# Kernel optimization log

Measured on AMD Instinct MI355X. Metric: run time of the kernel, lower is better.

## Reference

```python
import jax, jax.numpy as jnp
import numpy as np

NUM_NODES = 1_000_000
MEM_DIM = 100
TIME_DIM = 100
MSG_DIM = 4
OUT_CH = 2
BATCH = 262144
BN_EPS = 1e-5


def setup_inputs() -> dict:
    key = jax.random.key(0)
    ks = jax.random.split(key, 24)
    s = 0.05
    D = MEM_DIM
    gru_in = 2 * D + MSG_DIM + TIME_DIM  # IdentityMessage output dim = 304
    inp = {
        "n_id": jax.random.randint(ks[0], (BATCH,), 0, NUM_NODES, dtype=jnp.int64 if jax.config.jax_enable_x64 else jnp.int32),
        "memory": jax.random.normal(ks[1], (NUM_NODES, D), jnp.float32),
        "last_update": jax.random.randint(ks[2], (NUM_NODES,), 0, 100000),
        "store_src": jax.random.randint(ks[3], (NUM_NODES,), 0, NUM_NODES),
        "store_dst": jax.random.randint(ks[4], (NUM_NODES,), 0, NUM_NODES),
        "store_t": jax.random.randint(ks[5], (NUM_NODES,), 0, 200000),
        "store_msg": jax.random.normal(ks[6], (NUM_NODES, MSG_DIM), jnp.float32),
        # TimeEncoder: Linear(1, time_dim) followed by cos
        "time_w": jax.random.normal(ks[7], (TIME_DIM, 1), jnp.float32) * s,
        "time_b": jax.random.normal(ks[8], (TIME_DIM,), jnp.float32) * s,
        # GRUCell(input=304, hidden=100)
        "W_ih": jax.random.normal(ks[9], (3 * D, gru_in), jnp.float32) * s,
        "b_ih": jax.random.normal(ks[10], (3 * D,), jnp.float32) * s,
        "W_hh": jax.random.normal(ks[11], (3 * D, D), jnp.float32) * s,
        "b_hh": jax.random.normal(ks[12], (3 * D,), jnp.float32) * s,
        # classifier: Linear(100,64) -> ReLU -> BatchNorm1d(64) -> Linear(64,2)
        "W1": jax.random.normal(ks[13], (64, D), jnp.float32) * s,
        "b1": jax.random.normal(ks[14], (64,), jnp.float32) * s,
        "gamma": jnp.ones((64,), jnp.float32),
        "beta": jnp.zeros((64,), jnp.float32),
        "W2": jax.random.normal(ks[15], (OUT_CH, 64), jnp.float32) * s,
        "b2": jax.random.normal(ks[16], (OUT_CH,), jnp.float32) * s,
    }
    return inp


def reference(n_id, memory, last_update, store_src, store_dst, store_t, store_msg,
              time_w, time_b, W_ih, b_ih, W_hh, b_hh, W1, b1, gamma, beta, W2, b2):
    D = memory.shape[1]
    # ---- TGNMemory._get_updated_memory(n_id) with LastAggregator ----
    h = memory[n_id]                                   # [B, D] gather of node memory
    src = store_src[n_id]
    dst = store_dst[n_id]
    raw_msg = store_msg[n_id]                          # [B, msg_dim]
    dt = (store_t[n_id] - last_update[n_id]).astype(jnp.float32)[:, None]  # [B, 1]
    t_enc = jnp.cos(dt @ time_w.T + time_b)            # [B, time_dim]
    # IdentityMessage: concat(mem[src], mem[dst], raw_msg, time_enc)
    x = jnp.concatenate([memory[src], memory[dst], raw_msg, t_enc], axis=-1)  # [B, 2D+msg+T]
    # GRUCell update
    gi = x @ W_ih.T + b_ih                             # [B, 3D]
    gh = h @ W_hh.T + b_hh                             # [B, 3D]
    i_r, i_z, i_n = gi[:, :D], gi[:, D:2 * D], gi[:, 2 * D:]
    h_r, h_z, h_n = gh[:, :D], gh[:, D:2 * D], gh[:, 2 * D:]
    r = jax.nn.sigmoid(i_r + h_r)
    z = jax.nn.sigmoid(i_z + h_z)
    n = jnp.tanh(i_n + r * h_n)
    h_new = (1.0 - z) * n + z * h                      # [B, D]
    # ---- classifier: Linear -> ReLU -> BatchNorm1d (train stats) -> Linear ----
    a = jax.nn.relu(h_new @ W1.T + b1)                 # [B, 64]
    mu = jnp.mean(a, axis=0)
    var = jnp.var(a, axis=0)
    a = (a - mu) * jax.lax.rsqrt(var + BN_EPS) * gamma + beta
    return a @ W2.T + b2                               # [B, out_channels]
```

## Files before the change

### kernel.cpp

```cpp
#include <hip/hip_runtime.h>
#include <stdint.h>

#define BATCH   262144
#define DMEM    100
#define AS      456

typedef float    f32x4 __attribute__((ext_vector_type(4)));
typedef _Float16 f16x8 __attribute__((ext_vector_type(8)));
typedef unsigned short u16x4 __attribute__((ext_vector_type(4)));

__device__ __forceinline__ unsigned short f2h(float f) {
  union { _Float16 h; unsigned short u; } v; v.h = (_Float16)f;
  return v.u;
}
__device__ __forceinline__ float h2f(unsigned short u) {
  union { _Float16 h; unsigned short u; } v; v.u = u; return (float)v.h;
}

#define MFMA16(A, B, C) __builtin_amdgcn_mfma_f32_16x16x32_f16((A), (B), (C), 0, 0, 0)

__global__ void prep_kernel(const float* __restrict__ W_ih, const float* __restrict__ W_hh,
                            const float* __restrict__ W1,
                            const float* __restrict__ b_ih, const float* __restrict__ b_hh,
                            unsigned short* __restrict__ Bfrag,
                            unsigned short* __restrict__ W1frag,
                            float* __restrict__ biasbuf,
                            float* __restrict__ stats_g) {
  int blk = blockIdx.x;
  int tid = threadIdx.x;
  if (blk == 72) {
    if (tid < 128) stats_g[tid] = 0.f;
    if (tid < 100) {
      biasbuf[tid]       = b_ih[tid]       + b_hh[tid];
      biasbuf[100 + tid] = b_ih[100 + tid] + b_hh[100 + tid];
      biasbuf[200 + tid] = b_ih[200 + tid];
      biasbuf[300 + tid] = b_hh[200 + tid];
    }
    return;
  }
  int o = blk * 4 + (tid >> 6);
  if (o >= 286) return;
  int lane = tid & 63, quad = lane >> 4, l15 = lane & 15;
  if (o < 270) {
    int kc, nt;
    if (o < 190) { kc = o / 19; nt = o % 19; }
    else { int o2 = o - 190; kc = 10 + o2 / 20; int p = o2 % 20; nt = (p < 13) ? p : p + 6; }
    int col = nt * 16 + l15;
    unsigned short* dst = Bfrag + (size_t)o * 512 + lane * 8;
    for (int j = 0; j < 8; ++j) {
      int kg = kc * 32 + quad * 8 + j;
      float v = 0.f;
      if (kc < 10) {
        if (kg < 304 && col < 300) v = W_ih[col * 304 + kg];
      } else {
        int kl = kg - 320;
        if (nt < 13) { if (kl < 100 && col < 200) v = W_hh[col * 100 + kl]; }
        else { int hd = col - 304; if (kl < 100 && hd < 100) v = W_hh[(200 + hd) * 100 + kl]; }
      }
      dst[j] = f2h(v);
    }
  } else {
    int o1 = o - 270;
    int kc = o1 >> 2, nt = o1 & 3;
    int col = nt * 16 + l15;
    unsigned short* dst = W1frag + (size_t)o1 * 512 + lane * 8;
    for (int j = 0; j < 8; ++j) {
      int kg = kc * 32 + quad * 8 + j;
      dst[j] = f2h((kg < 100) ? W1[col * 100 + kg] : 0.f);
    }
  }
}

__global__ __launch_bounds__(256, 2)
void main_kernel(const int* __restrict__ n_id, const float* __restrict__ memory,
                 const int* __restrict__ last_update,
                 const int* __restrict__ store_src, const int* __restrict__ store_dst,
                 const int* __restrict__ store_t, const float* __restrict__ store_msg,
                 const float* __restrict__ time_w, const float* __restrict__ time_b,
                 const float* __restrict__ b1,
                 const unsigned short* __restrict__ Bfrag,
                 const unsigned short* __restrict__ W1frag,
                 const float* __restrict__ biasbuf,
                 unsigned short* __restrict__ a_ws, float* __restrict__ stats_g) {
  __shared__ __align__(16) unsigned short A_lds[64 * AS];
  __shared__ __align__(16) unsigned short hbuf[64 * 100];
  __shared__ float stats[128];

  const int tid  = threadIdx.x;
  const int wave = tid >> 6;
  const int lane = tid & 63;
  const int quad = lane >> 4;
  const int l15  = lane & 15;
  const int wi   = wave >> 1;
  const int wj   = wave & 1;
  const int blk  = blockIdx.x;

  if (tid < 128) stats[tid] = 0.f;

  {
    const int r = tid >> 2;
    const int p = tid & 3;
    const int b = blk * 64 + r;
    const int n = n_id[b];
    const int sidx = store_src[n];
    const int didx = store_dst[n];
    const float dtf = (float)(store_t[n] - last_update[n]);
    const float* ms = memory + (size_t)sidx * DMEM;
    const float* md = memory + (size_t)didx * DMEM;
    const float* mh = memory + (size_t)n * DMEM;
    unsigned short* Ar = A_lds + r * AS;

    f32x4 vals[19];
    int   offs[19];
    #pragma unroll
    for (int i = 0; i < 19; ++i) {
      const int v = i * 4 + p;
      const int a = v / 25;
      const int c = v - a * 25;
      const float* bp = (a == 0) ? ms : ((a == 1) ? md : mh);
      vals[i] = *(const f32x4*)(bp + c * 4);
      offs[i] = (a == 0) ? (c * 4)
              : ((a == 1) ? (100 + c * 4)
              : ((a == 2) ? (320 + c * 4) : 448));
    }
    #pragma unroll
    for (int i = 0; i < 19; ++i) {
      u16x4 h4 = { f2h(vals[i][0]), f2h(vals[i][1]), f2h(vals[i][2]), f2h(vals[i][3]) };
      *(u16x4*)(Ar + offs[i]) = h4;
    }

    const int d0 = p * 25;
    for (int i = 0; i < 25; ++i) {
      const int d = d0 + i;
      Ar[204 + d] = f2h(cosf(dtf * time_w[d] + time_b[d]));
    }

    if (p == 0) {
      f32x4 mg = *(const f32x4*)(store_msg + (size_t)n * 4);
      u16x4 m4 = { f2h(mg[0]), f2h(mg[1]), f2h(mg[2]), f2h(mg[3]) };
      *(u16x4*)(Ar + 200) = m4;
    } else if (p == 1) {
      uint4 z4 = {0u, 0u, 0u, 0u};
      *(uint4*)(Ar + 304) = z4;
      *(uint4*)(Ar + 312) = z4;
    } else if (p == 2) {
      u16x4 z = {0, 0, 0, 0};
      *(u16x4*)(Ar + 420) = z; *(u16x4*)(Ar + 424) = z;
      *(u16x4*)(Ar + 428) = z; *(u16x4*)(Ar + 432) = z;
    } else {
      u16x4 z = {0, 0, 0, 0};
      *(u16x4*)(Ar + 436) = z; *(u16x4*)(Ar + 440) = z; *(u16x4*)(Ar + 444) = z;
    }
  }

  f32x4 acc[13][2];
  #pragma unroll
  for (int t = 0; t < 13; ++t)
    for (int m = 0; m < 2; ++m) acc[t][m] = f32x4{0.f, 0.f, 0.f, 0.f};

  __syncthreads();

  const unsigned short* Arow0 = A_lds + (wi * 32 + l15) * AS;
  const unsigned short* Arow1 = Arow0 + 16 * AS;
  const size_t boff = (size_t)lane * 8;

  if (wj == 0) {
    #pragma unroll 2
    for (int kc = 0; kc < 10; ++kc) {
      const int kb = kc * 32 + quad * 8;
      f16x8 af0 = __builtin_bit_cast(f16x8, *(const uint4*)(Arow0 + kb));
      f16x8 af1 = __builtin_bit_cast(f16x8, *(const uint4*)(Arow1 + kb));
      const unsigned short* Bp = Bfrag + (size_t)(kc * 19) * 512 + boff;
      #pragma unroll
      for (int t = 0; t < 10; ++t) {
        f16x8 bfr = *(const f16x8*)(Bp + (size_t)(2 * t) * 512);
        acc[t][0] = MFMA16(af0, bfr, acc[t][0]);
        acc[t][1] = MFMA16(af1, bfr, acc[t][1]);
      }
    }
    #pragma unroll 2
    for (int kc = 10; kc < 14; ++kc) {
      const int kb = kc * 32 + quad * 8;
      f16x8 af0 = __builtin_bit_cast(f16x8, *(const uint4*)(Arow0 + kb));
      f16x8 af1 = __builtin_bit_cast(f16x8, *(const uint4*)(Arow1 + kb));
      const unsigned short* Bp = Bfrag + (size_t)(190 + (kc - 10) * 20) * 512 + boff;
      #pragma unroll
      for (int t = 0; t < 10; ++t) {
        const int p  = 2 * t;
        const int tl = (p < 13) ? (p >> 1) : ((p + 6) >> 1);
        f16x8 bfr = *(const f16x8*)(Bp + (size_t)p * 512);
        acc[tl][0] = MFMA16(af0, bfr, acc[tl][0]);
        acc[tl][1] = MFMA16(af1, bfr, acc[tl][1]);
      }
    }
  } else {
    #pragma unroll 2
    for (int kc = 0; kc < 10; ++kc) {
      const int kb = kc * 32 + quad * 8;
      f16x8 af0 = __builtin_bit_cast(f16x8, *(const uint4*)(Arow0 + kb));
      f16x8 af1 = __builtin_bit_cast(f16x8, *(const uint4*)(Arow1 + kb));
      const unsigned short* Bp = Bfrag + (size_t)(kc * 19) * 512 + boff;
      #pragma unroll
      for (int t = 0; t < 9; ++t) {
        f16x8 bfr = *(const f16x8*)(Bp + (size_t)(2 * t + 1) * 512);
        acc[t][0] = MFMA16(af0, bfr, acc[t][0]);
        acc[t][1] = MFMA16(af1, bfr, acc[t][1]);
      }
    }
    #pragma unroll 2
    for (int kc = 10; kc < 14; ++kc) {
      const int kb = kc * 32 + quad * 8;
      f16x8 af0 = __builtin_bit_cast(f16x8, *(const uint4*)(Arow0 + kb));
      f16x8 af1 = __builtin_bit_cast(f16x8, *(const uint4*)(Arow1 + kb));
      const unsigned short* Bp = Bfrag + (size_t)(190 + (kc - 10) * 20) * 512 + boff;
      #pragma unroll
      for (int t = 0; t < 10; ++t) {
        const int p  = 2 * t + 1;
        const int tl = (p < 13) ? (p >> 1) : ((p + 6) >> 1);
        f16x8 bfr = *(const f16x8*)(Bp + (size_t)p * 512);
        acc[tl][0] = MFMA16(af0, bfr, acc[tl][0]);
        acc[tl][1] = MFMA16(af1, bfr, acc[tl][1]);
      }
    }
  }
  __syncthreads();

  for (int i = 0; i < 25; ++i) {
    int e = tid + 256 * i;
    hbuf[e] = A_lds[(e / 100) * AS + 320 + (e % 100)];
  }
  __syncthreads();

  #pragma unroll
  for (int t = 0; t < 13; ++t) {
    int col = (t * 2 + wj) * 16 + l15;
    #pragma unroll
    for (int m = 0; m < 2; ++m) {
      int rbase = wi * 32 + m * 16 + quad * 4;
      #pragma unroll
      for (int rr = 0; rr < 4; ++rr)
        A_lds[(rbase + rr) * AS + col] = f2h(acc[t][m][rr]);
    }
  }
  __syncthreads();

  for (int i = 0; i < 25; ++i) {
    int e = tid + 256 * i;
    int r = e / 100, d = e % 100;
    const unsigned short* Gr = A_lds + r * AS;
    float s_r = h2f(Gr[d])       + biasbuf[d];
    float s_z = h2f(Gr[100 + d]) + biasbuf[100 + d];
    float i_n = h2f(Gr[200 + d]) + biasbuf[200 + d];
    float h_n = h2f(Gr[304 + d]) + biasbuf[300 + d];
    float h   = h2f(hbuf[r * 100 + d]);
    float rg = 1.f / (1.f + __expf(-s_r));
    float zg = 1.f / (1.f + __expf(-s_z));
    float nn = tanhf(i_n + rg * h_n);
    float hw = (1.f - zg) * nn + zg * h;
    A_lds[r * AS + d] = f2h(hw);
  }
  __syncthreads();

  f32x4 aacc[2][2];
  #pragma unroll
  for (int m = 0; m < 2; ++m)
    for (int t = 0; t < 2; ++t) aacc[m][t] = f32x4{0.f, 0.f, 0.f, 0.f};
  for (int k4 = 0; k4 < 4; ++k4) {
    int kb = k4 * 32 + quad * 8;
    f16x8 a0 = __builtin_bit_cast(f16x8, *(const uint4*)(Arow0 + kb));
    f16x8 a1 = __builtin_bit_cast(f16x8, *(const uint4*)(Arow1 + kb));
    #pragma unroll
    for (int t = 0; t < 2; ++t) {
      int nt = wj * 2 + t;
      f16x8 bfr = *(const f16x8*)(W1frag + (size_t)(k4 * 4 + nt) * 512 + boff);
      aacc[0][t] = MFMA16(a0, bfr, aacc[0][t]);
      aacc[1][t] = MFMA16(a1, bfr, aacc[1][t]);
    }
  }

  float ssum[2] = {0.f, 0.f}, ssq[2] = {0.f, 0.f};
  #pragma unroll
  for (int t = 0; t < 2; ++t) {
    int col = (wj * 2 + t) * 16 + l15;
    float bb = b1[col];
    #pragma unroll
    for (int m = 0; m < 2; ++m) {
      int rbase = wi * 32 + m * 16 + quad * 4;
      #pragma unroll
      for (int rr = 0; rr < 4; ++rr) {
        float v = fmaxf(aacc[m][t][rr] + bb, 0.f);
        ssum[t] += v; ssq[t] += v * v;
        a_ws[(size_t)(blk * 64 + rbase + rr) * 64 + col] = f2h(v);
      }
    }
  }
  #pragma unroll
  for (int t = 0; t < 2; ++t) {
    ssum[t] += __shfl_xor(ssum[t], 16); ssum[t] += __shfl_xor(ssum[t], 32);
    ssq[t]  += __shfl_xor(ssq[t], 16);  ssq[t]  += __shfl_xor(ssq[t], 32);
  }
  if (quad == 0) {
    #pragma unroll
    for (int t = 0; t < 2; ++t) {
      int col = (wj * 2 + t) * 16 + l15;
      atomicAdd(&stats[col], ssum[t]);
      atomicAdd(&stats[64 + col], ssq[t]);
    }
  }
  __syncthreads();
  if (tid < 128) atomicAdd(&stats_g[tid], stats[tid]);
}

__global__ __launch_bounds__(256)
void out_kernel(const unsigned short* __restrict__ a_ws, const float* __restrict__ stats_g,
                const float* __restrict__ gamma, const float* __restrict__ beta,
                const float* __restrict__ W2, const float* __restrict__ b2,
                float* __restrict__ out) {
  __shared__ float w0[64], w1[64], cpart[128];
  __shared__ float C0s, C1s;
  int tid = threadIdx.x;
  if (tid < 64) {
    const float invB = 1.f / (float)BATCH;
    float mu  = stats_g[tid] * invB;
    float var = stats_g[64 + tid] * invB - mu * mu;
    float g   = gamma[tid] * rsqrtf(var + 1e-5f);
    w0[tid] = g * W2[tid];
    w1[tid] = g * W2[64 + tid];
    float t = beta[tid] - mu * g;
    cpart[tid]      = t * W2[tid];
    cpart[64 + tid] = t * W2[64 + tid];
  }
  __syncthreads();
  if (tid == 0) {
    float c0 = b2[0], c1 = b2[1];
    for (int j = 0; j < 64; ++j) { c0 += cpart[j]; c1 += cpart[64 + j]; }
    C0s = c0; C1s = c1;
  }
  __syncthreads();
  int b = blockIdx.x * 256 + tid;
  const uint4* ap = (const uint4*)(a_ws + (size_t)b * 64);
  float o0 = C0s, o1 = C1s;
  #pragma unroll
  for (int i = 0; i < 8; ++i) {
    uint4 v = ap[i];
    unsigned int uu[4] = {v.x, v.y, v.z, v.w};
    #pragma unroll
    for (int q = 0; q < 4; ++q) {
      float lo = h2f((unsigned short)(uu[q] & 0xffffu));
      float hi = h2f((unsigned short)(uu[q] >> 16));
      int j = i * 8 + q * 2;
      o0 += lo * w0[j] + hi * w0[j + 1];
      o1 += lo * w1[j] + hi * w1[j + 1];
    }
  }
  *(float2*)(out + (size_t)b * 2) = make_float2(o0, o1);
}

extern "C" void kernel_launch(void* const* d_in, const int* in_sizes, int n_in,
                              void* d_out, int out_size, void* d_ws, size_t ws_size,
                              hipStream_t stream) {
  const int*   n_id   = (const int*)d_in[0];
  const float* memory = (const float*)d_in[1];
  const int*   last_u = (const int*)d_in[2];
  const int*   s_src  = (const int*)d_in[3];
  const int*   s_dst  = (const int*)d_in[4];
  const int*   s_t    = (const int*)d_in[5];
  const float* s_msg  = (const float*)d_in[6];
  const float* time_w = (const float*)d_in[7];
  const float* time_b = (const float*)d_in[8];
  const float* W_ih   = (const float*)d_in[9];
  const float* b_ih   = (const float*)d_in[10];
  const float* W_hh   = (const float*)d_in[11];
  const float* b_hh   = (const float*)d_in[12];
  const float* W1     = (const float*)d_in[13];
  const float* b1     = (const float*)d_in[14];
  const float* gamma  = (const float*)d_in[15];
  const float* beta   = (const float*)d_in[16];
  const float* W2     = (const float*)d_in[17];
  const float* b2     = (const float*)d_in[18];

  char* ws = (char*)d_ws;
  float*          stats_g = (float*)ws;
  float*          biasbuf = (float*)(ws + 512);
  unsigned short* Bfrag   = (unsigned short*)(ws + 4096);
  unsigned short* W1frag  = (unsigned short*)(ws + 4096 + 276480);
  unsigned short* a_ws    = (unsigned short*)(ws + (1u << 20));

  prep_kernel<<<73, 256, 0, stream>>>(W_ih, W_hh, W1, b_ih, b_hh, Bfrag, W1frag,
                                      biasbuf, stats_g);
  main_kernel<<<4096, 256, 0, stream>>>(n_id, memory, last_u, s_src, s_dst, s_t,
                                        s_msg, time_w, time_b, b1,
                                        Bfrag, W1frag, biasbuf, a_ws, stats_g);
  out_kernel<<<1024, 256, 0, stream>>>(a_ws, stats_g, gamma, beta, W2, b2, (float*)d_out);
}
```

Before: 829.5 us.

## Repartition GRU GEMM across waves by N-tiles with B-fragment register prefetch

Replaces the 2x2 wave tiling of the fused GRU GEMM with a per-wave set of N-tiles covering all 64 rows, so each A fragment is reused across 4 row tiles. B fragments are software-prefetched one K-chunk ahead in registers, and the classifier GEMM likewise gives each wave one output column tile with W1 fragments preloaded. Biases are staged in LDS, and tanh/sigmoid use fast exp plus reciprocal. The larger accumulator footprint (28 f32x4) and the prefetch buffers raise register pressure at 2 blocks per CU, and the wave load is uneven (one wave has 5 tiles).

```diff
diff --git a/kernel.cpp b/kernel.cpp
--- a/kernel.cpp
+++ b/kernel.cpp
@@ -18,6 +18,15 @@
 }
 
 #define MFMA16(A, B, C) __builtin_amdgcn_mfma_f32_16x16x32_f16((A), (B), (C), 0, 0, 0)
+
+namespace wcfg {
+constexpr int NT[4][7] = {
+  {0, 1, 2, 3, 19, 20, 21},
+  {4, 5, 6, 7, 22, 23, 24},
+  {8, 9, 10, 11, 13, 13, 13},
+  {12, 14, 15, 16, 17, 18, 25}};
+constexpr int LEN[4] = {7, 7, 5, 7};
+}
 
 __global__ void prep_kernel(const float* __restrict__ W_ih, const float* __restrict__ W_hh,
                             const float* __restrict__ W1,
@@ -71,6 +80,110 @@
   }
 }
 
+template<int W>
+__device__ __forceinline__ void b_prefetch0(f16x8 (&bq)[7],
+    const unsigned short* __restrict__ Bfrag, size_t boff) {
+  constexpr auto& NT = wcfg::NT[W];
+  constexpr int L = wcfg::LEN[W];
+  #pragma unroll
+  for (int t = 0; t < 7; ++t)
+    if (t < L && NT[t] < 19)
+      bq[t] = *(const f16x8*)(Bfrag + (size_t)NT[t] * 512 + boff);
+}
+
+template<int W>
+__device__ __forceinline__ void gemm_core(f32x4 (&acc)[7][4], f16x8 (&bq)[7],
+    const unsigned short* __restrict__ Bfrag, const unsigned short* Arow,
+    int quad, size_t boff) {
+  constexpr auto& NT = wcfg::NT[W];
+  constexpr int L = wcfg::LEN[W];
+  #pragma unroll
+  for (int kc = 0; kc < 10; ++kc) {
+    const int kb = kc * 32 + quad * 8;
+    f16x8 af[4];
+    #pragma unroll
+    for (int m = 0; m < 4; ++m)
+      af[m] = __builtin_bit_cast(f16x8, *(const uint4*)(Arow + m * 16 * AS + kb));
+    f16x8 bn[7];
+    if (kc < 9) {
+      const unsigned short* Bk = Bfrag + (size_t)(kc + 1) * 19 * 512 + boff;
+      #pragma unroll
+      for (int t = 0; t < 7; ++t)
+        if (t < L && NT[t] < 19)
+          bn[t] = *(const f16x8*)(Bk + (size_t)NT[t] * 512);
+    } else {
+      const unsigned short* Bk = Bfrag + (size_t)190 * 512 + boff;
+      #pragma unroll
+      for (int t = 0; t < 7; ++t)
+        if (t < L && (NT[t] < 13 || NT[t] >= 19))
+          bn[t] = *(const f16x8*)(Bk + (size_t)((NT[t] < 13) ? NT[t] : NT[t] - 6) * 512);
+    }
+    #pragma unroll
+    for (int t = 0; t < 7; ++t)
+      if (t < L && NT[t] < 19) {
+        #pragma unroll
+        for (int m = 0; m < 4; ++m)
+          acc[t][m] = MFMA16(af[m], bq[t], acc[t][m]);
+      }
+    if (kc < 9) {
+      #pragma unroll
+      for (int t = 0; t < 7; ++t)
+        if (t < L && NT[t] < 19) bq[t] = bn[t];
+    } else {
+      #pragma unroll
+      for (int t = 0; t < 7; ++t)
+        if (t < L && (NT[t] < 13 || NT[t] >= 19)) bq[t] = bn[t];
+    }
+  }
+  #pragma unroll
+  for (int kc = 10; kc < 14; ++kc) {
+    const int kb = kc * 32 + quad * 8;
+    f16x8 af[4];
+    #pragma unroll
+    for (int m = 0; m < 4; ++m)
+      af[m] = __builtin_bit_cast(f16x8, *(const uint4*)(Arow + m * 16 * AS + kb));
+    f16x8 bn[7];
+    if (kc < 13) {
+      const unsigned short* Bk = Bfrag + (size_t)(190 + (kc - 9) * 20) * 512 + boff;
+      #pragma unroll
+      for (int t = 0; t < 7; ++t)
+        if (t < L && (NT[t] < 13 || NT[t] >= 19))
+          bn[t] = *(const f16x8*)(Bk + (size_t)((NT[t] < 13) ? NT[t] : NT[t] - 6) * 512);
+    }
+    #pragma unroll
+    for (int t = 0; t < 7; ++t)
+      if (t < L && (NT[t] < 13 || NT[t] >= 19)) {
+        #pragma unroll
+        for (int m = 0; m < 4; ++m)
+          acc[t][m] = MFMA16(af[m], bq[t], acc[t][m]);
+      }
+    if (kc < 13) {
+      #pragma unroll
+      for (int t = 0; t < 7; ++t)
+        if (t < L && (NT[t] < 13 || NT[t] >= 19)) bq[t] = bn[t];
+    }
+  }
+}
+
+template<int W>
+__device__ __forceinline__ void dump_acc(const f32x4 (&acc)[7][4],
+    unsigned short* A_lds, int quad, int l15) {
+  constexpr auto& NT = wcfg::NT[W];
+  constexpr int L = wcfg::LEN[W];
+  #pragma unroll
+  for (int t = 0; t < 7; ++t)
+    if (t < L) {
+      const int col = NT[t] * 16 + l15;
+      #pragma unroll
+      for (int m = 0; m < 4; ++m) {
+        const int rbase = m * 16 + quad * 4;
+        #pragma unroll
+        for (int rr = 0; rr < 4; ++rr)
+          A_lds[(rbase + rr) * AS + col] = f2h(acc[t][m][rr]);
+      }
+    }
+}
+
 __global__ __launch_bounds__(256, 2)
 void main_kernel(const int* __restrict__ n_id, const float* __restrict__ memory,
                  const int* __restrict__ last_update,
@@ -84,6 +197,7 @@
                  unsigned short* __restrict__ a_ws, float* __restrict__ stats_g) {
   __shared__ __align__(16) unsigned short A_lds[64 * AS];
   __shared__ __align__(16) unsigned short hbuf[64 * 100];
+  __shared__ float bias_lds[400];
   __shared__ float stats[128];
 
   const int tid  = threadIdx.x;
@@ -91,11 +205,14 @@
   const int lane = tid & 63;
   const int quad = lane >> 4;
   const int l15  = lane & 15;
-  const int wi   = wave >> 1;
-  const int wj   = wave & 1;
   const int blk  = blockIdx.x;
+  const size_t boff = (size_t)lane * 8;
 
   if (tid < 128) stats[tid] = 0.f;
+  if (tid < 200) {
+    bias_lds[tid]       = biasbuf[tid];
+    bias_lds[200 + tid] = biasbuf[200 + tid];
+  }
 
   {
     const int r = tid >> 2;
@@ -104,14 +221,14 @@
     const int n = n_id[b];
     const int sidx = store_src[n];
     const int didx = store_dst[n];
-    const float dtf = (float)(store_t[n] - last_update[n]);
+    const int stt  = store_t[n];
+    const int lu   = last_update[n];
     const float* ms = memory + (size_t)sidx * DMEM;
     const float* md = memory + (size_t)didx * DMEM;
     const float* mh = memory + (size_t)n * DMEM;
     unsigned short* Ar = A_lds + r * AS;
 
     f32x4 vals[19];
-    int   offs[19];
     #pragma unroll
     for (int i = 0; i < 19; ++i) {
       const int v = i * 4 + p;
@@ -119,24 +236,17 @@
       const int c = v - a * 25;
       const float* bp = (a == 0) ? ms : ((a == 1) ? md : mh);
       vals[i] = *(const f32x4*)(bp + c * 4);
-      offs[i] = (a == 0) ? (c * 4)
-              : ((a == 1) ? (100 + c * 4)
-              : ((a == 2) ? (320 + c * 4) : 448));
-    }
-    #pragma unroll
-    for (int i = 0; i < 19; ++i) {
-      u16x4 h4 = { f2h(vals[i][0]), f2h(vals[i][1]), f2h(vals[i][2]), f2h(vals[i][3]) };
-      *(u16x4*)(Ar + offs[i]) = h4;
-    }
-
+    }
+    f32x4 mg;
+    if (p == 0) mg = *(const f32x4*)(store_msg + (size_t)n * 4);
+
+    const float dtf = (float)(stt - lu);
     const int d0 = p * 25;
     for (int i = 0; i < 25; ++i) {
       const int d = d0 + i;
       Ar[204 + d] = f2h(cosf(dtf * time_w[d] + time_b[d]));
     }
-
     if (p == 0) {
-      f32x4 mg = *(const f32x4*)(store_msg + (size_t)n * 4);
       u16x4 m4 = { f2h(mg[0]), f2h(mg[1]), f2h(mg[2]), f2h(mg[3]) };
       *(u16x4*)(Ar + 200) = m4;
     } else if (p == 1) {
@@ -151,77 +261,40 @@
       u16x4 z = {0, 0, 0, 0};
       *(u16x4*)(Ar + 436) = z; *(u16x4*)(Ar + 440) = z; *(u16x4*)(Ar + 444) = z;
     }
-  }
-
-  f32x4 acc[13][2];
-  #pragma unroll
-  for (int t = 0; t < 13; ++t)
-    for (int m = 0; m < 2; ++m) acc[t][m] = f32x4{0.f, 0.f, 0.f, 0.f};
-
-  __syncthreads();
-
-  const unsigned short* Arow0 = A_lds + (wi * 32 + l15) * AS;
-  const unsigned short* Arow1 = Arow0 + 16 * AS;
-  const size_t boff = (size_t)lane * 8;
-
-  if (wj == 0) {
-    #pragma unroll 2
-    for (int kc = 0; kc < 10; ++kc) {
-      const int kb = kc * 32 + quad * 8;
-      f16x8 af0 = __builtin_bit_cast(f16x8, *(const uint4*)(Arow0 + kb));
-      f16x8 af1 = __builtin_bit_cast(f16x8, *(const uint4*)(Arow1 + kb));
-      const unsigned short* Bp = Bfrag + (size_t)(kc * 19) * 512 + boff;
-      #pragma unroll
-      for (int t = 0; t < 10; ++t) {
-        f16x8 bfr = *(const f16x8*)(Bp + (size_t)(2 * t) * 512);
-        acc[t][0] = MFMA16(af0, bfr, acc[t][0]);
-        acc[t][1] = MFMA16(af1, bfr, acc[t][1]);
-      }
-    }
-    #pragma unroll 2
-    for (int kc = 10; kc < 14; ++kc) {
-      const int kb = kc * 32 + quad * 8;
-      f16x8 af0 = __builtin_bit_cast(f16x8, *(const uint4*)(Arow0 + kb));
-      f16x8 af1 = __builtin_bit_cast(f16x8, *(const uint4*)(Arow1 + kb));
-      const unsigned short* Bp = Bfrag + (size_t)(190 + (kc - 10) * 20) * 512 + boff;
-      #pragma unroll
-      for (int t = 0; t < 10; ++t) {
-        const int p  = 2 * t;
-        const int tl = (p < 13) ? (p >> 1) : ((p + 6) >> 1);
-        f16x8 bfr = *(const f16x8*)(Bp + (size_t)p * 512);
-        acc[tl][0] = MFMA16(af0, bfr, acc[tl][0]);
-        acc[tl][1] = MFMA16(af1, bfr, acc[tl][1]);
-      }
-    }
-  } else {
-    #pragma unroll 2
-    for (int kc = 0; kc < 10; ++kc) {
-      const int kb = kc * 32 + quad * 8;
-      f16x8 af0 = __builtin_bit_cast(f16x8, *(const uint4*)(Arow0 + kb));
-      f16x8 af1 = __builtin_bit_cast(f16x8, *(const uint4*)(Arow1 + kb));
-      const unsigned short* Bp = Bfrag + (size_t)(kc * 19) * 512 + boff;
-      #pragma unroll
-      for (int t = 0; t < 9; ++t) {
-        f16x8 bfr = *(const f16x8*)(Bp + (size_t)(2 * t + 1) * 512);
-        acc[t][0] = MFMA16(af0, bfr, acc[t][0]);
-        acc[t][1] = MFMA16(af1, bfr, acc[t][1]);
-      }
-    }
-    #pragma unroll 2
-    for (int kc = 10; kc < 14; ++kc) {
-      const int kb = kc * 32 + quad * 8;
-      f16x8 af0 = __builtin_bit_cast(f16x8, *(const uint4*)(Arow0 + kb));
-      f16x8 af1 = __builtin_bit_cast(f16x8, *(const uint4*)(Arow1 + kb));
-      const unsigned short* Bp = Bfrag + (size_t)(190 + (kc - 10) * 20) * 512 + boff;
-      #pragma unroll
-      for (int t = 0; t < 10; ++t) {
-        const int p  = 2 * t + 1;
-        const int tl = (p < 13) ? (p >> 1) : ((p + 6) >> 1);
-        f16x8 bfr = *(const f16x8*)(Bp + (size_t)p * 512);
-        acc[tl][0] = MFMA16(af0, bfr, acc[tl][0]);
-        acc[tl][1] = MFMA16(af1, bfr, acc[tl][1]);
-      }
-    }
+    #pragma unroll
+    for (int i = 0; i < 19; ++i) {
+      const int v = i * 4 + p;
+      const int a = v / 25;
+      const int c = v - a * 25;
+      const int off = (a == 0) ? (c * 4)
+                    : ((a == 1) ? (100 + c * 4)
+                    : ((a == 2) ? (320 + c * 4) : 448));
+      u16x4 h4 = { f2h(vals[i][0]), f2h(vals[i][1]), f2h(vals[i][2]), f2h(vals[i][3]) };
+      *(u16x4*)(Ar + off) = h4;
+    }
+  }
+
+  f32x4 acc[7][4];
+  #pragma unroll
+  for (int t = 0; t < 7; ++t)
+    #pragma unroll
+    for (int m = 0; m < 4; ++m) acc[t][m] = f32x4{0.f, 0.f, 0.f, 0.f};
+
+  f16x8 bq[7];
+  switch (wave) {
+    case 0: b_prefetch0<0>(bq, Bfrag, boff); break;
+    case 1: b_prefetch0<1>(bq, Bfrag, boff); break;
+    case 2: b_prefetch0<2>(bq, Bfrag, boff); break;
+    default: b_prefetch0<3>(bq, Bfrag, boff); break;
+  }
+  __syncthreads();
+
+  const unsigned short* Arow = A_lds + l15 * AS;
+  switch (wave) {
+    case 0: gemm_core<0>(acc, bq, Bfrag, Arow, quad, boff); break;
+    case 1: gemm_core<1>(acc, bq, Bfrag, Arow, quad, boff); break;
+    case 2: gemm_core<2>(acc, bq, Bfrag, Arow, quad, boff); break;
+    default: gemm_core<3>(acc, bq, Bfrag, Arow, quad, boff); break;
   }
   __syncthreads();
 
@@ -231,81 +304,71 @@
   }
   __syncthreads();
 
-  #pragma unroll
-  for (int t = 0; t < 13; ++t) {
-    int col = (t * 2 + wj) * 16 + l15;
-    #pragma unroll
-    for (int m = 0; m < 2; ++m) {
-      int rbase = wi * 32 + m * 16 + quad * 4;
-      #pragma unroll
-      for (int rr = 0; rr < 4; ++rr)
-        A_lds[(rbase + rr) * AS + col] = f2h(acc[t][m][rr]);
-    }
-  }
+  switch (wave) {
+    case 0: dump_acc<0>(acc, A_lds, quad, l15); break;
+    case 1: dump_acc<1>(acc, A_lds, quad, l15); break;
+    case 2: dump_acc<2>(acc, A_lds, quad, l15); break;
+    default: dump_acc<3>(acc, A_lds, quad, l15); break;
+  }
+
+  f16x8 wb[4];
+  #pragma unroll
+  for (int k4 = 0; k4 < 4; ++k4)
+    wb[k4] = *(const f16x8*)(W1frag + (size_t)(k4 * 4 + wave) * 512 + boff);
+
   __syncthreads();
 
   for (int i = 0; i < 25; ++i) {
     int e = tid + 256 * i;
     int r = e / 100, d = e % 100;
     const unsigned short* Gr = A_lds + r * AS;
-    float s_r = h2f(Gr[d])       + biasbuf[d];
-    float s_z = h2f(Gr[100 + d]) + biasbuf[100 + d];
-    float i_n = h2f(Gr[200 + d]) + biasbuf[200 + d];
-    float h_n = h2f(Gr[304 + d]) + biasbuf[300 + d];
+    float s_r = h2f(Gr[d])       + bias_lds[d];
+    float s_z = h2f(Gr[100 + d]) + bias_lds[100 + d];
+    float i_n = h2f(Gr[200 + d]) + bias_lds[200 + d];
+    float h_n = h2f(Gr[304 + d]) + bias_lds[300 + d];
     float h   = h2f(hbuf[r * 100 + d]);
-    float rg = 1.f / (1.f + __expf(-s_r));
-    float zg = 1.f / (1.f + __expf(-s_z));
-    float nn = tanhf(i_n + rg * h_n);
+    float rg = __builtin_amdgcn_rcpf(1.f + __expf(-s_r));
+    float zg = __builtin_amdgcn_rcpf(1.f + __expf(-s_z));
+    float x2 = i_n + rg * h_n;
+    x2 = fminf(fmaxf(x2, -30.f), 30.f);
+    float e2 = __expf(-2.f * x2);
+    float nn = (1.f - e2) * __builtin_amdgcn_rcpf(1.f + e2);
     float hw = (1.f - zg) * nn + zg * h;
     A_lds[r * AS + d] = f2h(hw);
   }
   __syncthreads();
 
-  f32x4 aacc[2][2];
-  #pragma unroll
-  for (int m = 0; m < 2; ++m)
-    for (int t = 0; t < 2; ++t) aacc[m][t] = f32x4{0.f, 0.f, 0.f, 0.f};
+  f32x4 aacc[4];
+  #pragma unroll
+  for (int m = 0; m < 4; ++m) aacc[m] = f32x4{0.f, 0.f, 0.f, 0.f};
+  #pragma unroll
   for (int k4 = 0; k4 < 4; ++k4) {
-    int kb = k4 * 32 + quad * 8;
-    f16x8 a0 = __builtin_bit_cast(f16x8, *(const uint4*)(Arow0 + kb));
-    f16x8 a1 = __builtin_bit_cast(f16x8, *(const uint4*)(Arow1 + kb));
-    #pragma unroll
-    for (int t = 0; t < 2; ++t) {
-      int nt = wj * 2 + t;
-      f16x8 bfr = *(const f16x8*)(W1frag + (size_t)(k4 * 4 + nt) * 512 + boff);
-      aacc[0][t] = MFMA16(a0, bfr, aacc[0][t]);
-      aacc[1][t] = MFMA16(a1, bfr, aacc[1][t]);
-    }
-  }
-
-  float ssum[2] = {0.f, 0.f}, ssq[2] = {0.f, 0.f};
-  #pragma unroll
-  for (int t = 0; t < 2; ++t) {
-    int col = (wj * 2 + t) * 16 + l15;
-    float bb = b1[col];
-    #pragma unroll
-    for (int m = 0; m < 2; ++m) {
-      int rbase = wi * 32 + m * 16 + quad * 4;
-      #pragma unroll
-      for (int rr = 0; rr < 4; ++rr) {
-        float v = fmaxf(aacc[m][t][rr] + bb, 0.f);
-        ssum[t] += v; ssq[t] += v * v;
-        a_ws[(size_t)(blk * 64 + rbase + rr) * 64 + col] = f2h(v);
-      }
-    }
-  }
-  #pragma unroll
-  for (int t = 0; t < 2; ++t) {
-    ssum[t] += __shfl_xor(ssum[t], 16); ssum[t] += __shfl_xor(ssum[t], 32);
-    ssq[t]  += __shfl_xor(ssq[t], 16);  ssq[t]  += __shfl_xor(ssq[t], 32);
-  }
+    const int kb = k4 * 32 + quad * 8;
+    #pragma unroll
+    for (int m = 0; m < 4; ++m) {
+      f16x8 a = __builtin_bit_cast(f16x8, *(const uint4*)(Arow + m * 16 * AS + kb));
+      aacc[m] = MFMA16(a, wb[k4], aacc[m]);
+    }
+  }
+
+  const int col = wave * 16 + l15;
+  const float bb = b1[col];
+  float ssum = 0.f, ssq = 0.f;
+  #pragma unroll
+  for (int m = 0; m < 4; ++m) {
+    const int rbase = m * 16 + quad * 4;
+    #pragma unroll
+    for (int rr = 0; rr < 4; ++rr) {
+      float v = fmaxf(aacc[m][rr] + bb, 0.f);
+      ssum += v; ssq += v * v;
+      a_ws[(size_t)(blk * 64 + rbase + rr) * 64 + col] = f2h(v);
+    }
+  }
+  ssum += __shfl_xor(ssum, 16); ssum += __shfl_xor(ssum, 32);
+  ssq  += __shfl_xor(ssq, 16);  ssq  += __shfl_xor(ssq, 32);
   if (quad == 0) {
-    #pragma unroll
-    for (int t = 0; t < 2; ++t) {
-      int col = (wj * 2 + t) * 16 + l15;
-      atomicAdd(&stats[col], ssum[t]);
-      atomicAdd(&stats[64 + col], ssq[t]);
-    }
+    atomicAdd(&stats[col], ssum);
+    atomicAdd(&stats[64 + col], ssq);
   }
   __syncthreads();
   if (tid < 128) atomicAdd(&stats_g[tid], stats[tid]);
```

Result: faster. 749.9 us (-9.6%).
